# Kernel tuning notes

Measured on AMD Instinct MI355X. Metric: run time of the kernel, lower is better.

The kernel has to match this reference:

```python
import jax, jax.numpy as jnp
import numpy as np

N_HEADS = 16


def setup_inputs() -> dict:
    key = jax.random.key(0)
    k1, k2 = jax.random.split(key)
    bs, width, length = 8, 3 * N_HEADS * 64, 1024  # C=64 per head
    qkv = jax.random.normal(k1, (bs, width, length), dtype=jnp.float32)
    mask = jax.random.uniform(k2, (bs, length), dtype=jnp.float32)
    return {"qkv": qkv, "mask": mask}


def reference(qkv, mask):
    bs, width, length = qkv.shape
    ch = width // (3 * N_HEADS)
    q, k, v = jnp.split(qkv, 3, axis=1)
    # view(bs*H, ch, T): head index is inner (b*H + h ordering)
    q = q.reshape(bs * N_HEADS, ch, length)
    k = k.reshape(bs * N_HEADS, ch, length)
    v = v.reshape(bs * N_HEADS, ch, length)
    scale = 1.0 / jnp.sqrt(jnp.sqrt(jnp.asarray(ch, dtype=qkv.dtype)))
    # [bs*H, T, T] score matrix
    weight = jnp.einsum('bct,bcs->bts', q * scale, k * scale)
    # torch mask.repeat(n_heads, 1) tiles the batch dim -> jnp.tile
    m = jnp.tile(mask, (N_HEADS, 1))[:, None, :]  # [bs*H, 1, T]
    weight = weight * m
    weight = jax.nn.softmax(weight.astype(jnp.float32), axis=-1).astype(weight.dtype)
    a = jnp.einsum('bts,bcs->bct', weight, v)  # [bs*H, ch, T]
    return a.reshape(bs, N_HEADS * ch, length)
```

## Files before the change

kernel.cpp:

```cpp
#include <hip/hip_runtime.h>
#include <stdint.h>
#include <math.h>

typedef float  f32x4  __attribute__((ext_vector_type(4)));
typedef __bf16 bf16x8 __attribute__((ext_vector_type(8)));
typedef __bf16 bf16x4 __attribute__((ext_vector_type(4)));

#define MFMA16(a, b, c) __builtin_amdgcn_mfma_f32_16x16x32_bf16((a), (b), (c), 0, 0, 0)
#define EXP2(x) __builtin_amdgcn_exp2f(x)

static constexpr int kT    = 1024;
static constexpr int kLS   = 72;
static constexpr int kTile = 64 * kLS;
static constexpr size_t kTensorEl    = (size_t)128 * 16 * kTile;
static constexpr size_t kTensorBytes = kTensorEl * 2;

__device__ inline void async16(const void* g, void* l) {
  __builtin_amdgcn_global_load_lds(
      (const __attribute__((address_space(1))) void*)g,
      (__attribute__((address_space(3))) void*)l, 16, 0, 0);
}

__global__ __launch_bounds__(256, 8)
void prepass(const float* __restrict__ qkv, const float* __restrict__ mask,
             __bf16* __restrict__ kh, __bf16* __restrict__ vh)
{
  __shared__ float ts[64 * 65];
  const int tid = threadIdx.x;
  const int bid = blockIdx.x, bh = bid >> 4, tile = bid & 15;
  const int b = bh >> 4, h = bh & 15, t0 = tile * 64;
  const float* __restrict__ kb = qkv + (size_t)(b * 3072 + 1024 + h * 64) * kT;
  const float* __restrict__ vb = qkv + (size_t)(b * 3072 + 2048 + h * 64) * kT;
  const float* __restrict__ mrow = mask + (size_t)(h & 7) * kT;
  const size_t tbase = ((size_t)bh * 16 + tile) * kTile;

  const int t4   = (tid & 15) * 4;
  const int crow = tid >> 4;
  const f32x4 m4 = *(const f32x4*)&mrow[t0 + t4];

  #pragma unroll
  for (int i = 0; i < 4; ++i) {
    const int c = i * 16 + crow;
    f32x4 k4 = *(const f32x4*)&kb[(size_t)c * kT + t0 + t4];
    k4 *= m4;
    *(f32x4*)&ts[c * 65 + t4] = k4;
    f32x4 v4 = *(const f32x4*)&vb[(size_t)c * kT + t0 + t4];
    bf16x4 v4h;
    #pragma unroll
    for (int j = 0; j < 4; ++j) v4h[j] = (__bf16)v4[j];
    *(bf16x4*)&vh[tbase + c * kLS + t4] = v4h;
  }
  __syncthreads();

  const int c0 = tid & 15;
  const int rr = tid >> 4;
  #pragma unroll
  for (int i = 0; i < 4; ++i) {
    const int row = i * 16 + rr;
    bf16x4 kh4;
    #pragma unroll
    for (int j = 0; j < 4; ++j) kh4[j] = (__bf16)ts[(c0 * 4 + j) * 65 + row];
    *(bf16x4*)&kh[tbase + row * kLS + c0 * 4] = kh4;
  }
}

__global__ __launch_bounds__(256, 4)
void attn_main(const float* __restrict__ qkv,
               const __bf16* __restrict__ kh, const __bf16* __restrict__ vh,
               float* __restrict__ out)
{
  __shared__ __align__(16) __bf16 sK[2][kTile];
  __shared__ __align__(16) __bf16 sP[128 * kLS];

  const int tid  = threadIdx.x;
  const int lane = tid & 63;
  const int wave = tid >> 6;
  const int quad = lane >> 4;
  const int l15  = lane & 15;

  const int bid = blockIdx.x;
  const int bh  = bid & 127;
  const int tp  = bid >> 7;
  const int b   = bh >> 4;
  const int h   = bh & 15;
  const int t0  = tp * 128;

  const size_t hbase = (size_t)bh * 16;

  bf16x8 ones8;
  #pragma unroll
  for (int j = 0; j < 8; ++j) ones8[j] = (__bf16)1.0f;

  int ro[4];
  #pragma unroll
  for (int i = 0; i < 4; ++i) ro[i] = (i * 16 + l15) * kLS + quad * 8;

  bf16x8 qhf[2][2], qlf[2][2];
  {
    float* ts = (float*)sK;
    const float* __restrict__ qb = qkv + (size_t)(b * 3072 + h * 64) * kT;
    const int t4   = (tid & 15) * 4;
    const int crow = tid >> 4;
    const int trow = wave * 16 + l15;
    #pragma unroll
    for (int half = 0; half < 2; ++half) {
      const int tq0 = t0 + half * 64;
      #pragma unroll
      for (int i = 0; i < 4; ++i) {
        const int c = i * 16 + crow;
        f32x4 q4 = *(const f32x4*)&qb[(size_t)c * kT + tq0 + t4];
        q4 *= 0.18033688f;
        *(f32x4*)&ts[c * 65 + t4] = q4;
      }
      __syncthreads();
      #pragma unroll
      for (int kc = 0; kc < 2; ++kc) {
        bf16x8 hf, lf;
        #pragma unroll
        for (int j = 0; j < 8; ++j) {
          float q = ts[(kc * 32 + quad * 8 + j) * 65 + trow];
          __bf16 hi = (__bf16)q;
          hf[j] = hi;
          lf[j] = (__bf16)(q - (float)hi);
        }
        qhf[half][kc] = hf;
        qlf[half][kc] = lf;
      }
      __syncthreads();
    }
  }

  {
    const char* g = (const char*)(kh + hbase * kTile) + (size_t)lane * 16;
    char* l = (char*)sK[0];
    for (int i = wave; i < 9; i += 4) async16(g + i * 1024, l + i * 1024);
  }

  f32x4 O0[4], O1[4];
  #pragma unroll
  for (int cc = 0; cc < 4; ++cc) {
    O0[cc] = (f32x4){0.f, 0.f, 0.f, 0.f};
    O1[cc] = (f32x4){0.f, 0.f, 0.f, 0.f};
  }
  f32x4 L0 = (f32x4){0.f, 0.f, 0.f, 0.f};
  f32x4 L1 = (f32x4){0.f, 0.f, 0.f, 0.f};

  const int pw0 = (wave * 32 + l15) * kLS;
  const int pw1 = pw0 + 16 * kLS;

  for (int st = 0; st < 16; ++st) {
    __syncthreads();

    const __bf16* __restrict__ vb = vh + (hbase + st) * kTile;

    bf16x8 vf0[4];
    #pragma unroll
    for (int cc = 0; cc < 4; ++cc) vf0[cc] = *(const bf16x8*)&vb[ro[cc]];

    if (st < 15) {
      const char* g = (const char*)(kh + (hbase + st + 1) * kTile) + (size_t)lane * 16;
      char* l = (char*)sK[(st + 1) & 1];
      for (int i = wave; i < 9; i += 4) async16(g + i * 1024, l + i * 1024);
    }

    const __bf16* __restrict__ sKc = sK[st & 1];

    #pragma unroll
    for (int sc = 0; sc < 4; ++sc) {
      bf16x8 k0 = *(const bf16x8*)&sKc[ro[sc]];
      bf16x8 k1 = *(const bf16x8*)&sKc[ro[sc] + 32];
      f32x4 a0 = (f32x4){0.f, 0.f, 0.f, 0.f};
      f32x4 a1 = (f32x4){0.f, 0.f, 0.f, 0.f};
      a0 = MFMA16(k0, qlf[0][0], a0);
      a0 = MFMA16(k0, qhf[0][0], a0);
      a0 = MFMA16(k1, qlf[0][1], a0);
      a0 = MFMA16(k1, qhf[0][1], a0);
      a1 = MFMA16(k0, qlf[1][0], a1);
      a1 = MFMA16(k0, qhf[1][0], a1);
      a1 = MFMA16(k1, qlf[1][1], a1);
      a1 = MFMA16(k1, qhf[1][1], a1);
      bf16x4 p0, p1;
      #pragma unroll
      for (int r = 0; r < 4; ++r) {
        p0[r] = (__bf16)EXP2(a0[r]);
        p1[r] = (__bf16)EXP2(a1[r]);
      }
      *(bf16x4*)&sP[pw0 + sc * 16 + quad * 4] = p0;
      *(bf16x4*)&sP[pw1 + sc * 16 + quad * 4] = p1;
    }

    bf16x8 vf1[4];
    #pragma unroll
    for (int cc = 0; cc < 4; ++cc) vf1[cc] = *(const bf16x8*)&vb[ro[cc] + 32];

    bf16x8 pb0[2], pb1[2];
    #pragma unroll
    for (int kc = 0; kc < 2; ++kc) {
      pb0[kc] = *(const bf16x8*)&sP[pw0 + kc * 32 + quad * 8];
      pb1[kc] = *(const bf16x8*)&sP[pw1 + kc * 32 + quad * 8];
    }
    L0 = MFMA16(ones8, pb0[0], L0);
    L0 = MFMA16(ones8, pb0[1], L0);
    L1 = MFMA16(ones8, pb1[0], L1);
    L1 = MFMA16(ones8, pb1[1], L1);

    #pragma unroll
    for (int cc = 0; cc < 4; ++cc) {
      O0[cc] = MFMA16(vf0[cc], pb0[0], O0[cc]);
      O0[cc] = MFMA16(vf1[cc], pb0[1], O0[cc]);
      O1[cc] = MFMA16(vf0[cc], pb1[0], O1[cc]);
      O1[cc] = MFMA16(vf1[cc], pb1[1], O1[cc]);
    }
  }

  const float inv0 = 1.0f / L0[0];
  const float inv1 = 1.0f / L1[0];
  const int tcol = t0 + wave * 16 + l15;
  float* __restrict__ obase = out + (size_t)b * (1024 * 1024) + (size_t)(h * 64) * kT;
  #pragma unroll
  for (int cc = 0; cc < 4; ++cc) {
    #pragma unroll
    for (int r = 0; r < 4; ++r) {
      const int c = cc * 16 + quad * 4 + r;
      obase[(size_t)c * kT + tcol]      = O0[cc][r] * inv0;
      obase[(size_t)c * kT + tcol + 64] = O1[cc][r] * inv1;
    }
  }
}

__global__ __launch_bounds__(256, 2)
void attn_fused(const float* __restrict__ qkv, const float* __restrict__ mask,
                float* __restrict__ out)
{
  __shared__ __align__(16) __bf16 Ahi[64 * kLS];
  __shared__ __align__(16) __bf16 Alo[64 * kLS];
  __shared__ __align__(16) __bf16 Vhi[64 * kLS];
  __shared__ __align__(16) __bf16 Vlo[64 * kLS];
  __shared__ __align__(16) __bf16 Phi[64 * kLS];
  __shared__ __align__(16) __bf16 Plo[64 * kLS];
  __shared__ __align__(16) float  ms[64];

  const int tid  = threadIdx.x;
  const int lane = tid & 63;
  const int wave = tid >> 6;
  const int quad = lane >> 4;
  const int l15  = lane & 15;

  const int bid = blockIdx.x;
  const int bh  = bid >> 4;
  const int tb  = bid & 15;
  const int b   = bh >> 4;
  const int h   = bh & 15;
  const int t0  = tb * 64;

  const float* __restrict__ qbase = qkv + (size_t)(b * 3072 + h * 64) * kT;
  const float* __restrict__ kbase = qkv + (size_t)(b * 3072 + 1024 + h * 64) * kT;
  const float* __restrict__ vbase = qkv + (size_t)(b * 3072 + 2048 + h * 64) * kT;
  const float* __restrict__ mrow  = mask + (size_t)(h & 7) * kT;

  const int sl = tid & 63;
  const int cg = tid >> 6;

  #pragma unroll
  for (int i = 0; i < 16; ++i) {
    const int c = cg * 16 + i;
    float v  = qbase[(size_t)c * kT + t0 + sl] * 0.125f;
    __bf16 hi = (__bf16)v;
    Ahi[sl * kLS + c] = hi;
    Alo[sl * kLS + c] = (__bf16)(v - (float)hi);
  }
  __syncthreads();

  bf16x8 qh[2], ql[2];
  {
    const int row = (wave * 16 + l15) * kLS;
    #pragma unroll
    for (int kc = 0; kc < 2; ++kc) {
      qh[kc] = *(const bf16x8*)&Ahi[row + kc * 32 + quad * 8];
      ql[kc] = *(const bf16x8*)&Alo[row + kc * 32 + quad * 8];
    }
  }
  __syncthreads();

  f32x4 O[4];
  #pragma unroll
  for (int cc = 0; cc < 4; ++cc) O[cc] = (f32x4){0.f, 0.f, 0.f, 0.f};
  float m_run = -__builtin_inff();
  float l_run = 0.f;

  for (int s0 = 0; s0 < kT; s0 += 64) {
    #pragma unroll
    for (int i = 0; i < 16; ++i) {
      const int c = cg * 16 + i;
      float kv   = kbase[(size_t)c * kT + s0 + sl];
      __bf16 khi = (__bf16)kv;
      Ahi[sl * kLS + c] = khi;
      Alo[sl * kLS + c] = (__bf16)(kv - (float)khi);
      float vv   = vbase[(size_t)c * kT + s0 + sl];
      __bf16 vhi = (__bf16)vv;
      Vhi[c * kLS + sl] = vhi;
      Vlo[c * kLS + sl] = (__bf16)(vv - (float)vhi);
    }
    if (tid < 64) ms[tid] = mrow[s0 + tid];
    __syncthreads();

    f32x4 S[4];
    #pragma unroll
    for (int sc = 0; sc < 4; ++sc) {
      f32x4 acc = (f32x4){0.f, 0.f, 0.f, 0.f};
      #pragma unroll
      for (int kc = 0; kc < 2; ++kc) {
        const int off = (sc * 16 + l15) * kLS + kc * 32 + quad * 8;
        bf16x8 kh8 = *(const bf16x8*)&Ahi[off];
        bf16x8 kl8 = *(const bf16x8*)&Alo[off];
        acc = MFMA16(kh8, ql[kc], acc);
        acc = MFMA16(kl8, qh[kc], acc);
        acc = MFMA16(kh8, qh[kc], acc);
      }
      S[sc] = acc;
    }

    float x[16];
    float tmax = -__builtin_inff();
    #pragma unroll
    for (int sc = 0; sc < 4; ++sc) {
      f32x4 mv = *(const f32x4*)&ms[sc * 16 + quad * 4];
      #pragma unroll
      for (int r = 0; r < 4; ++r) {
        float xv = S[sc][r] * mv[r];
        x[sc * 4 + r] = xv;
        tmax = fmaxf(tmax, xv);
      }
    }
    tmax = fmaxf(tmax, __shfl_xor(tmax, 16));
    tmax = fmaxf(tmax, __shfl_xor(tmax, 32));
    const float mnew  = fmaxf(m_run, tmax);
    const float alpha = __expf(m_run - mnew);
    float tsum = 0.f;
    #pragma unroll
    for (int i = 0; i < 16; ++i) {
      float p = __expf(x[i] - mnew);
      x[i] = p;
      tsum += p;
    }
    tsum += __shfl_xor(tsum, 16);
    tsum += __shfl_xor(tsum, 32);
    l_run = l_run * alpha + tsum;
    m_run = mnew;
    #pragma unroll
    for (int cc = 0; cc < 4; ++cc) O[cc] = O[cc] * alpha;

    const int prow = (wave * 16 + l15) * kLS;
    #pragma unroll
    for (int sc = 0; sc < 4; ++sc) {
      bf16x4 ph, pl;
      #pragma unroll
      for (int r = 0; r < 4; ++r) {
        float p   = x[sc * 4 + r];
        __bf16 hi = (__bf16)p;
        ph[r] = hi;
        pl[r] = (__bf16)(p - (float)hi);
      }
      *(bf16x4*)&Phi[prow + sc * 16 + quad * 4] = ph;
      *(bf16x4*)&Plo[prow + sc * 16 + quad * 4] = pl;
    }
    __syncthreads();

    bf16x8 pbh[2], pbl[2];
    #pragma unroll
    for (int kc = 0; kc < 2; ++kc) {
      pbh[kc] = *(const bf16x8*)&Phi[prow + kc * 32 + quad * 8];
      pbl[kc] = *(const bf16x8*)&Plo[prow + kc * 32 + quad * 8];
    }
    #pragma unroll
    for (int cc = 0; cc < 4; ++cc) {
      #pragma unroll
      for (int kc = 0; kc < 2; ++kc) {
        const int off = (cc * 16 + l15) * kLS + kc * 32 + quad * 8;
        bf16x8 v8 = *(const bf16x8*)&Vhi[off];
        bf16x8 w8 = *(const bf16x8*)&Vlo[off];
        O[cc] = MFMA16(v8, pbl[kc], O[cc]);
        O[cc] = MFMA16(w8, pbh[kc], O[cc]);
        O[cc] = MFMA16(v8, pbh[kc], O[cc]);
      }
    }
    __syncthreads();
  }

  const float inv  = 1.0f / l_run;
  const int   tcol = t0 + wave * 16 + l15;
  float* __restrict__ obase = out + (size_t)b * (1024 * 1024) + (size_t)(h * 64) * kT;
  #pragma unroll
  for (int cc = 0; cc < 4; ++cc) {
    #pragma unroll
    for (int r = 0; r < 4; ++r) {
      const int c = cc * 16 + quad * 4 + r;
      obase[(size_t)c * kT + tcol] = O[cc][r] * inv;
    }
  }
}

extern "C" void kernel_launch(void* const* d_in, const int* in_sizes, int n_in,
                              void* d_out, int out_size, void* d_ws, size_t ws_size,
                              hipStream_t stream)
{
  const float* qkv  = (const float*)d_in[0];
  const float* mask = (const float*)d_in[1];
  float* out = (float*)d_out;
  (void)in_sizes; (void)n_in; (void)out_size;

  if (ws_size >= 2 * kTensorBytes) {
    char* w = (char*)d_ws;
    __bf16* kh = (__bf16*)(w + 0 * kTensorBytes);
    __bf16* vh = (__bf16*)(w + 1 * kTensorBytes);
    prepass<<<dim3(2048), dim3(256), 0, stream>>>(qkv, mask, kh, vh);
    attn_main<<<dim3(1024), dim3(256), 0, stream>>>(qkv, kh, vh, out);
  } else {
    attn_fused<<<dim3(2048), dim3(256), 0, stream>>>(qkv, mask, out);
  }
}
```

Baseline: 210.7 us.

## Pre-swizzle K/V tiles into MFMA fragment order and halve query tile per block

The prepass now writes K and V tiles in unpadded 4096-element blocks already arranged in MFMA fragment order, so the main kernel reads each fragment with one contiguous 16-byte-per-lane load. attn_main drops from 128 to 64 queries per block, launches twice as many blocks, and raises the occupancy hint from 4 to 5. The row-sum now accumulates in registers with shuffles instead of extra MFMAs against a ones vector. Smaller tiles reduce per-block LDS and registers to improve latency hiding, but K/V tiles are reloaded twice as often per head.

```diff
diff --git a/kernel.cpp b/kernel.cpp
--- a/kernel.cpp
+++ b/kernel.cpp
@@ -9,11 +9,13 @@
 #define MFMA16(a, b, c) __builtin_amdgcn_mfma_f32_16x16x32_bf16((a), (b), (c), 0, 0, 0)
 #define EXP2(x) __builtin_amdgcn_exp2f(x)
 
-static constexpr int kT    = 1024;
-static constexpr int kLS   = 72;
-static constexpr int kTile = 64 * kLS;
-static constexpr size_t kTensorEl    = (size_t)128 * 16 * kTile;
+static constexpr int kT = 1024;
+
+static constexpr int kTileEl = 4096;
+static constexpr size_t kTensorEl    = (size_t)128 * 16 * kTileEl;
 static constexpr size_t kTensorBytes = kTensorEl * 2;
+
+static constexpr int kLS = 72;
 
 __device__ inline void async16(const void* g, void* l) {
   __builtin_amdgcn_global_load_lds(
@@ -32,45 +34,46 @@
   const float* __restrict__ kb = qkv + (size_t)(b * 3072 + 1024 + h * 64) * kT;
   const float* __restrict__ vb = qkv + (size_t)(b * 3072 + 2048 + h * 64) * kT;
   const float* __restrict__ mrow = mask + (size_t)(h & 7) * kT;
-  const size_t tbase = ((size_t)bh * 16 + tile) * kTile;
+  const size_t tbase = ((size_t)bh * 16 + tile) * kTileEl;
 
   const int t4   = (tid & 15) * 4;
   const int crow = tid >> 4;
   const f32x4 m4 = *(const f32x4*)&mrow[t0 + t4];
-
   #pragma unroll
   for (int i = 0; i < 4; ++i) {
     const int c = i * 16 + crow;
     f32x4 k4 = *(const f32x4*)&kb[(size_t)c * kT + t0 + t4];
     k4 *= m4;
     *(f32x4*)&ts[c * 65 + t4] = k4;
-    f32x4 v4 = *(const f32x4*)&vb[(size_t)c * kT + t0 + t4];
-    bf16x4 v4h;
-    #pragma unroll
-    for (int j = 0; j < 4; ++j) v4h[j] = (__bf16)v4[j];
-    *(bf16x4*)&vh[tbase + c * kLS + t4] = v4h;
   }
   __syncthreads();
 
-  const int c0 = tid & 15;
-  const int rr = tid >> 4;
-  #pragma unroll
-  for (int i = 0; i < 4; ++i) {
-    const int row = i * 16 + rr;
-    bf16x4 kh4;
-    #pragma unroll
-    for (int j = 0; j < 4; ++j) kh4[j] = (__bf16)ts[(c0 * 4 + j) * 65 + row];
-    *(bf16x4*)&kh[tbase + row * kLS + c0 * 4] = kh4;
-  }
-}
-
-__global__ __launch_bounds__(256, 4)
+  #pragma unroll
+  for (int i = 0; i < 2; ++i) {
+    const int p = i * 256 + tid;
+    const int chunk = p >> 6, pl = p & 63;
+    const int vc  = (chunk >> 1) * 16 + (pl & 15);
+    const int vs0 = (chunk & 1) * 32 + (pl >> 4) * 8;
+    const f32x4 va  = *(const f32x4*)&vb[(size_t)vc * kT + t0 + vs0];
+    const f32x4 vbq = *(const f32x4*)&vb[(size_t)vc * kT + t0 + vs0 + 4];
+    const int ks  = (chunk >> 1) * 16 + (pl & 15);
+    const int kc0 = (chunk & 1) * 32 + (pl >> 4) * 8;
+    bf16x8 k8, v8;
+    #pragma unroll
+    for (int j = 0; j < 8; ++j) k8[j] = (__bf16)ts[(kc0 + j) * 65 + ks];
+    #pragma unroll
+    for (int j = 0; j < 4; ++j) { v8[j] = (__bf16)va[j]; v8[4 + j] = (__bf16)vbq[j]; }
+    *(bf16x8*)&kh[tbase + (size_t)p * 8] = k8;
+    *(bf16x8*)&vh[tbase + (size_t)p * 8] = v8;
+  }
+}
+
+__global__ __launch_bounds__(256, 5)
 void attn_main(const float* __restrict__ qkv,
                const __bf16* __restrict__ kh, const __bf16* __restrict__ vh,
                float* __restrict__ out)
 {
-  __shared__ __align__(16) __bf16 sK[2][kTile];
-  __shared__ __align__(16) __bf16 sP[128 * kLS];
+  __shared__ __align__(16) char smem[24576];
 
   const int tid  = threadIdx.x;
   const int lane = tid & 63;
@@ -80,150 +83,118 @@
 
   const int bid = blockIdx.x;
   const int bh  = bid & 127;
-  const int tp  = bid >> 7;
+  const int tt  = bid >> 7;
   const int b   = bh >> 4;
   const int h   = bh & 15;
-  const int t0  = tp * 128;
-
+  const int t0  = tt * 64;
   const size_t hbase = (size_t)bh * 16;
 
-  bf16x8 ones8;
-  #pragma unroll
-  for (int j = 0; j < 8; ++j) ones8[j] = (__bf16)1.0f;
-
-  int ro[4];
-  #pragma unroll
-  for (int i = 0; i < 4; ++i) ro[i] = (i * 16 + l15) * kLS + quad * 8;
-
-  bf16x8 qhf[2][2], qlf[2][2];
+  bf16x8 qh[2], ql[2];
   {
-    float* ts = (float*)sK;
+    float* ts = (float*)smem;
     const float* __restrict__ qb = qkv + (size_t)(b * 3072 + h * 64) * kT;
     const int t4   = (tid & 15) * 4;
     const int crow = tid >> 4;
+    #pragma unroll
+    for (int i = 0; i < 4; ++i) {
+      const int c = i * 16 + crow;
+      f32x4 q4 = *(const f32x4*)&qb[(size_t)c * kT + t0 + t4];
+      q4 *= 0.18033688f;
+      *(f32x4*)&ts[c * 65 + t4] = q4;
+    }
+    __syncthreads();
     const int trow = wave * 16 + l15;
     #pragma unroll
-    for (int half = 0; half < 2; ++half) {
-      const int tq0 = t0 + half * 64;
-      #pragma unroll
-      for (int i = 0; i < 4; ++i) {
-        const int c = i * 16 + crow;
-        f32x4 q4 = *(const f32x4*)&qb[(size_t)c * kT + tq0 + t4];
-        q4 *= 0.18033688f;
-        *(f32x4*)&ts[c * 65 + t4] = q4;
-      }
-      __syncthreads();
-      #pragma unroll
-      for (int kc = 0; kc < 2; ++kc) {
-        bf16x8 hf, lf;
-        #pragma unroll
-        for (int j = 0; j < 8; ++j) {
-          float q = ts[(kc * 32 + quad * 8 + j) * 65 + trow];
-          __bf16 hi = (__bf16)q;
-          hf[j] = hi;
-          lf[j] = (__bf16)(q - (float)hi);
-        }
-        qhf[half][kc] = hf;
-        qlf[half][kc] = lf;
-      }
-      __syncthreads();
-    }
+    for (int kc = 0; kc < 2; ++kc) {
+      bf16x8 hf, lf;
+      #pragma unroll
+      for (int j = 0; j < 8; ++j) {
+        float q = ts[(kc * 32 + quad * 8 + j) * 65 + trow];
+        __bf16 hi = (__bf16)q;
+        hf[j] = hi;
+        lf[j] = (__bf16)(q - (float)hi);
+      }
+      qh[kc] = hf;
+      ql[kc] = lf;
+    }
+    __syncthreads();
   }
 
   {
-    const char* g = (const char*)(kh + hbase * kTile) + (size_t)lane * 16;
-    char* l = (char*)sK[0];
-    for (int i = wave; i < 9; i += 4) async16(g + i * 1024, l + i * 1024);
-  }
-
-  f32x4 O0[4], O1[4];
-  #pragma unroll
-  for (int cc = 0; cc < 4; ++cc) {
-    O0[cc] = (f32x4){0.f, 0.f, 0.f, 0.f};
-    O1[cc] = (f32x4){0.f, 0.f, 0.f, 0.f};
-  }
-  f32x4 L0 = (f32x4){0.f, 0.f, 0.f, 0.f};
-  f32x4 L1 = (f32x4){0.f, 0.f, 0.f, 0.f};
-
-  const int pw0 = (wave * 32 + l15) * kLS;
-  const int pw1 = pw0 + 16 * kLS;
+    const char* g = (const char*)(kh + hbase * kTileEl) + (size_t)lane * 16;
+    for (int i = wave; i < 8; i += 4) async16(g + i * 1024, smem + i * 1024);
+  }
+
+  f32x4 O[4];
+  #pragma unroll
+  for (int cc = 0; cc < 4; ++cc) O[cc] = (f32x4){0.f, 0.f, 0.f, 0.f};
+  float lsum = 0.f;
+
+  char* sPw = smem + 16384 + wave * 2048;
+  const int pwr = (l15 << 4) + ((quad & 1) << 3) + ((quad >> 1) << 8);
 
   for (int st = 0; st < 16; ++st) {
     __syncthreads();
 
-    const __bf16* __restrict__ vb = vh + (hbase + st) * kTile;
-
-    bf16x8 vf0[4];
-    #pragma unroll
-    for (int cc = 0; cc < 4; ++cc) vf0[cc] = *(const bf16x8*)&vb[ro[cc]];
+    const __bf16* __restrict__ vt = vh + (hbase + st) * kTileEl;
+
+    bf16x8 vf0[4], vf1[4];
+    #pragma unroll
+    for (int cc = 0; cc < 4; ++cc)
+      vf0[cc] = *(const bf16x8*)&vt[(size_t)(cc * 2) * 512 + lane * 8];
 
     if (st < 15) {
-      const char* g = (const char*)(kh + (hbase + st + 1) * kTile) + (size_t)lane * 16;
-      char* l = (char*)sK[(st + 1) & 1];
-      for (int i = wave; i < 9; i += 4) async16(g + i * 1024, l + i * 1024);
-    }
-
-    const __bf16* __restrict__ sKc = sK[st & 1];
+      const char* g = (const char*)(kh + (hbase + st + 1) * kTileEl) + (size_t)lane * 16;
+      char* l = smem + ((st + 1) & 1) * 8192;
+      for (int i = wave; i < 8; i += 4) async16(g + i * 1024, l + i * 1024);
+    }
+
+    const __bf16* __restrict__ sKc = (const __bf16*)(smem + (st & 1) * 8192);
 
     #pragma unroll
     for (int sc = 0; sc < 4; ++sc) {
-      bf16x8 k0 = *(const bf16x8*)&sKc[ro[sc]];
-      bf16x8 k1 = *(const bf16x8*)&sKc[ro[sc] + 32];
-      f32x4 a0 = (f32x4){0.f, 0.f, 0.f, 0.f};
-      f32x4 a1 = (f32x4){0.f, 0.f, 0.f, 0.f};
-      a0 = MFMA16(k0, qlf[0][0], a0);
-      a0 = MFMA16(k0, qhf[0][0], a0);
-      a0 = MFMA16(k1, qlf[0][1], a0);
-      a0 = MFMA16(k1, qhf[0][1], a0);
-      a1 = MFMA16(k0, qlf[1][0], a1);
-      a1 = MFMA16(k0, qhf[1][0], a1);
-      a1 = MFMA16(k1, qlf[1][1], a1);
-      a1 = MFMA16(k1, qhf[1][1], a1);
-      bf16x4 p0, p1;
+      bf16x8 k0 = *(const bf16x8*)&sKc[(size_t)(sc * 2) * 512 + lane * 8];
+      bf16x8 k1 = *(const bf16x8*)&sKc[(size_t)(sc * 2 + 1) * 512 + lane * 8];
+      f32x4 a = (f32x4){0.f, 0.f, 0.f, 0.f};
+      a = MFMA16(k0, ql[0], a);
+      a = MFMA16(k0, qh[0], a);
+      a = MFMA16(k1, ql[1], a);
+      a = MFMA16(k1, qh[1], a);
+      bf16x4 p;
       #pragma unroll
       for (int r = 0; r < 4; ++r) {
-        p0[r] = (__bf16)EXP2(a0[r]);
-        p1[r] = (__bf16)EXP2(a1[r]);
-      }
-      *(bf16x4*)&sP[pw0 + sc * 16 + quad * 4] = p0;
-      *(bf16x4*)&sP[pw1 + sc * 16 + quad * 4] = p1;
-    }
-
-    bf16x8 vf1[4];
-    #pragma unroll
-    for (int cc = 0; cc < 4; ++cc) vf1[cc] = *(const bf16x8*)&vb[ro[cc] + 32];
-
-    bf16x8 pb0[2], pb1[2];
-    #pragma unroll
-    for (int kc = 0; kc < 2; ++kc) {
-      pb0[kc] = *(const bf16x8*)&sP[pw0 + kc * 32 + quad * 8];
-      pb1[kc] = *(const bf16x8*)&sP[pw1 + kc * 32 + quad * 8];
-    }
-    L0 = MFMA16(ones8, pb0[0], L0);
-    L0 = MFMA16(ones8, pb0[1], L0);
-    L1 = MFMA16(ones8, pb1[0], L1);
-    L1 = MFMA16(ones8, pb1[1], L1);
+        float e = EXP2(a[r]);
+        lsum += e;
+        p[r] = (__bf16)e;
+      }
+      *(bf16x4*)(sPw + (((sc >> 1) << 10) + ((sc & 1) << 9) + pwr)) = p;
+    }
+
+    #pragma unroll
+    for (int cc = 0; cc < 4; ++cc)
+      vf1[cc] = *(const bf16x8*)&vt[(size_t)(cc * 2 + 1) * 512 + lane * 8];
+
+    bf16x8 pb0 = *(const bf16x8*)(sPw + lane * 16);
+    bf16x8 pb1 = *(const bf16x8*)(sPw + 1024 + lane * 16);
 
     #pragma unroll
     for (int cc = 0; cc < 4; ++cc) {
-      O0[cc] = MFMA16(vf0[cc], pb0[0], O0[cc]);
-      O0[cc] = MFMA16(vf1[cc], pb0[1], O0[cc]);
-      O1[cc] = MFMA16(vf0[cc], pb1[0], O1[cc]);
-      O1[cc] = MFMA16(vf1[cc], pb1[1], O1[cc]);
-    }
-  }
-
-  const float inv0 = 1.0f / L0[0];
-  const float inv1 = 1.0f / L1[0];
+      O[cc] = MFMA16(vf0[cc], pb0, O[cc]);
+      O[cc] = MFMA16(vf1[cc], pb1, O[cc]);
+    }
+  }
+
+  lsum += __shfl_xor(lsum, 16);
+  lsum += __shfl_xor(lsum, 32);
+  const float inv = 1.0f / lsum;
+
   const int tcol = t0 + wave * 16 + l15;
   float* __restrict__ obase = out + (size_t)b * (1024 * 1024) + (size_t)(h * 64) * kT;
   #pragma unroll
   for (int cc = 0; cc < 4; ++cc) {
     #pragma unroll
     for (int r = 0; r < 4; ++r) {
-      const int c = cc * 16 + quad * 4 + r;
-      obase[(size_t)c * kT + tcol]      = O0[cc][r] * inv0;
-      obase[(size_t)c * kT + tcol + 64] = O1[cc][r] * inv1;
+      obase[(size_t)(cc * 16 + quad * 4 + r) * kT + tcol] = O[cc][r] * inv;
     }
   }
 }
@@ -414,7 +385,7 @@
     __bf16* kh = (__bf16*)(w + 0 * kTensorBytes);
     __bf16* vh = (__bf16*)(w + 1 * kTensorBytes);
     prepass<<<dim3(2048), dim3(256), 0, stream>>>(qkv, mask, kh, vh);
-    attn_main<<<dim3(1024), dim3(256), 0, stream>>>(qkv, kh, vh, out);
+    attn_main<<<dim3(2048), dim3(256), 0, stream>>>(qkv, kh, vh, out);
   } else {
     attn_fused<<<dim3(2048), dim3(256), 0, stream>>>(qkv, mask, out);
   }
```

After: 214.7 us. No clear change (+1.9%).
